# Kernel tuning notes

Hardware: AMD Instinct MI355X
Metric: run time of the kernel (lower is better)

Reference implementation:

```python
import jax, jax.numpy as jnp
import numpy as np

B, IN, H = 8192, 2048, 2048
EFF = IN + H  # self_recurrent concat of [x_t, state]


def setup_inputs() -> dict:
    key = jax.random.key(0)
    ks = jax.random.split(key, 6)
    s_in = 1.0 / np.sqrt(EFF).astype(np.float32)
    s_h = 1.0 / np.sqrt(H).astype(np.float32)
    return {
        "x_t": jax.random.normal(ks[0], (B, IN), jnp.float32),
        "state": jax.random.normal(ks[1], (B, H), jnp.float32),
        "Wc": jax.random.normal(ks[2], (EFF, H), jnp.float32) * s_in,
        "Uc": jax.random.normal(ks[3], (H, H), jnp.float32) * s_h,
        "bc": jnp.zeros((H,), jnp.float32),
        "Wg": jax.random.normal(ks[4], (EFF, H), jnp.float32) * s_in,
        "Ug": jax.random.normal(ks[5], (H, H), jnp.float32) * s_h,
        "bg": jnp.zeros((H,), jnp.float32),
        "log_step": jnp.zeros((H,), jnp.float32),  # dt_scale=1.0 -> no init shift
        "gamma": jnp.ones((H,), jnp.float32),
        "beta": jnp.zeros((H,), jnp.float32),
    }


def _layernorm(x, gamma, beta, eps=1e-5):
    mu = jnp.mean(x, axis=-1, keepdims=True)
    var = jnp.mean((x - mu) ** 2, axis=-1, keepdims=True)
    return (x - mu) * jax.lax.rsqrt(var + eps) * gamma + beta


def reference(x_t, state, Wc, Uc, bc, Wg, Ug, bg, log_step, gamma, beta):
    dt = 1.0  # step(dt=1.0) * dt_scale(1.0)
    xin = jnp.concatenate([x_t, state], axis=-1)        # [B, EFF], self_recurrent
    cand = jnp.tanh(xin @ Wc + state @ Uc + bc)          # candidate state [B, H]
    gate = jax.nn.sigmoid(xin @ Wg + state @ Ug + bg)    # input gate [B, H]
    tau = jnp.exp(log_step)                              # learned time constant
    alpha = jnp.exp(-dt / tau)                           # exp(-dt/tau) decay
    h_new = alpha * state + (1.0 - alpha) * gate * cand  # liquid gated update
    return _layernorm(h_new, gamma, beta)                # post-norm
```

## Files before the change

kernel.cpp:

```cpp
#include <hip/hip_runtime.h>
#include <hip/hip_bf16.h>
#include <cstdint>
#include <cstddef>

#define Bsz 8192
#define Hdim 2048
#define Kdim 4096
#define Nall 4096

#define BM 128
#define BN 64
#define BK 32

typedef __attribute__((ext_vector_type(8))) short short8;
typedef __attribute__((ext_vector_type(4))) short short4v;
typedef __attribute__((ext_vector_type(4))) float floatx4;

__device__ __forceinline__ short f2bf(float f) {
    unsigned u = __float_as_uint(f);
    unsigned r = (u + 0x7fffu + ((u >> 16) & 1u)) >> 16;
    return (short)(r & 0xffffu);
}

__device__ __forceinline__ float fast_tanh(float x) {
    float e = __expf(2.f * x);
    return 1.f - 2.f / (e + 1.f);
}
__device__ __forceinline__ float fast_sigmoid(float x) {
    return 1.f / (1.f + __expf(-x));
}

__device__ __forceinline__ void g2l16(const void* g, void* l) {
    __builtin_amdgcn_global_load_lds(
        (const __attribute__((address_space(1))) unsigned int*)g,
        (__attribute__((address_space(3))) unsigned int*)l,
        16, 0, 0);
}

__global__ __launch_bounds__(256) void build_wt(
    const float* __restrict__ Wc, const float* __restrict__ Uc,
    const float* __restrict__ Wg, const float* __restrict__ Ug,
    short* __restrict__ Wt)
{
    __shared__ float tile[32][33];
    const int nt = blockIdx.x * 32;
    const int kt = blockIdx.y * 32;
    const int tx = threadIdx.x & 31;
    const int ty = threadIdx.x >> 5;

    const bool isGate = (nt >= Hdim);
    const float* W = isGate ? Wg : Wc;
    const float* U = isGate ? Ug : Uc;
    const int ncol = isGate ? (nt - Hdim) : nt;

#pragma unroll
    for (int r = 0; r < 32; r += 8) {
        int k = kt + ty + r;
        float v = W[(size_t)k * Hdim + ncol + tx];
        if (k >= Hdim) v += U[(size_t)(k - Hdim) * Hdim + ncol + tx];
        tile[ty + r][tx] = v;
    }
    __syncthreads();
    const int nrow = threadIdx.x >> 3;
    const int kg   = threadIdx.x & 7;
    short4v o;
#pragma unroll
    for (int i = 0; i < 4; ++i) o[i] = f2bf(tile[kg * 4 + i][nrow]);
    *(short4v*)&Wt[(size_t)(nt + nrow) * Kdim + kt + kg * 4] = o;
}

__global__ __launch_bounds__(256) void build_acat(
    const float* __restrict__ x, const float* __restrict__ st,
    short* __restrict__ A)
{
    int idx = blockIdx.x * 256 + threadIdx.x;
    int row = idx >> 9;
    int c = (idx & 511) * 8;
    const float* src = (c < Hdim) ? (x + (size_t)row * Hdim + c)
                                  : (st + (size_t)row * Hdim + (c - Hdim));
    float4 v0 = ((const float4*)src)[0];
    float4 v1 = ((const float4*)src)[1];
    short8 o;
    o[0] = f2bf(v0.x); o[1] = f2bf(v0.y); o[2] = f2bf(v0.z); o[3] = f2bf(v0.w);
    o[4] = f2bf(v1.x); o[5] = f2bf(v1.y); o[6] = f2bf(v1.z); o[7] = f2bf(v1.w);
    *(short8*)(A + (size_t)row * Kdim + c) = o;
}

__global__ __launch_bounds__(256, 2) void gemm_fused(
    const short* __restrict__ A,
    const short* __restrict__ Bt,
    const float* __restrict__ st,
    const float* __restrict__ bc, const float* __restrict__ bg,
    const float* __restrict__ lstep,
    float* __restrict__ Hout)
{
    __shared__ __attribute__((aligned(16))) short sA [BM * BK];
    __shared__ __attribute__((aligned(16))) short sBc[BN * BK];
    __shared__ __attribute__((aligned(16))) short sBg[BN * BK];

    const int tid  = threadIdx.x;
    const int lane = tid & 63;
    const int wave = tid >> 6;
    const int wm = wave >> 1;
    const int wn = wave & 1;

    const int m0 = blockIdx.y * BM;
    const int n0 = blockIdx.x * BN;
    const int K = Kdim;

    floatx4 accc[4][2], accg[4][2];
#pragma unroll
    for (int i = 0; i < 4; ++i)
#pragma unroll
        for (int j = 0; j < 2; ++j) {
            floatx4 z = {0.f, 0.f, 0.f, 0.f};
            accc[i][j] = z; accg[i][j] = z;
        }

    const int r0 = tid >> 2;
    const int c0 = ((tid & 3) ^ ((r0 >> 1) & 3)) * 8;
    const short* Ag0 = A  + (size_t)(m0 + r0)        * K + c0;
    const short* Ag1 = A  + (size_t)(m0 + 64 + r0)   * K + c0;
    const short* Bc0 = Bt + (size_t)(n0 + r0)        * K + c0;
    const short* Bg0 = Bt + (size_t)(Hdim + n0 + r0) * K + c0;

    short* dA0 = sA  + wave * 512;
    short* dA1 = sA  + 2048 + wave * 512;
    short* dBc = sBc + wave * 512;
    short* dBg = sBg + wave * 512;

    const int fr = lane & 15;
    const int j4 = lane >> 4;
    const int rslot = (j4 ^ ((fr >> 1) & 3)) * 8;
    const short* sAf  = sA  + (wm * 64 + fr) * BK + rslot;
    const short* sBcf = sBc + (wn * 32 + fr) * BK + rslot;
    const short* sBgf = sBg + (wn * 32 + fr) * BK + rslot;

    for (int k0 = 0; k0 < K; k0 += BK) {
        __syncthreads();
        g2l16(Ag0, dA0); g2l16(Ag1, dA1);
        g2l16(Bc0, dBc); g2l16(Bg0, dBg);
        Ag0 += BK; Ag1 += BK; Bc0 += BK; Bg0 += BK;
        __syncthreads();

        short8 a[4], bcf[2], bgf[2];
#pragma unroll
        for (int i = 0; i < 4; ++i) a[i] = *(const short8*)(sAf + i * 16 * BK);
#pragma unroll
        for (int j = 0; j < 2; ++j) {
            bcf[j] = *(const short8*)(sBcf + j * 16 * BK);
            bgf[j] = *(const short8*)(sBgf + j * 16 * BK);
        }
#pragma unroll
        for (int i = 0; i < 4; ++i)
#pragma unroll
            for (int j = 0; j < 2; ++j) {
                accc[i][j] = __builtin_amdgcn_mfma_f32_16x16x32_bf16(
                    a[i], bcf[j], accc[i][j], 0, 0, 0);
                accg[i][j] = __builtin_amdgcn_mfma_f32_16x16x32_bf16(
                    a[i], bgf[j], accg[i][j], 0, 0, 0);
            }
    }

    const int cn = lane & 15;
    const int cr = (lane >> 4) * 4;
    float bcv[2], bgv[2], alv[2];
#pragma unroll
    for (int j = 0; j < 2; ++j) {
        int col = n0 + wn * 32 + j * 16 + cn;
        bcv[j] = bc[col];
        bgv[j] = bg[col];
        alv[j] = __expf(-__expf(-lstep[col]));
    }
#pragma unroll
    for (int i = 0; i < 4; ++i) {
        int rowb = m0 + wm * 64 + i * 16 + cr;
#pragma unroll
        for (int r = 0; r < 4; ++r) {
            int row = rowb + r;
            const float* sp = st + (size_t)row * Hdim;
            float* hp = Hout + (size_t)row * Hdim;
#pragma unroll
            for (int j = 0; j < 2; ++j) {
                int col = n0 + wn * 32 + j * 16 + cn;
                float cand = fast_tanh(accc[i][j][r] + bcv[j]);
                float gate = fast_sigmoid(accg[i][j][r] + bgv[j]);
                float al = alv[j];
                hp[col] = al * sp[col] + (1.f - al) * gate * cand;
            }
        }
    }
}

__global__ __launch_bounds__(256) void ln_k(
    const float* __restrict__ h, const float* __restrict__ gam,
    const float* __restrict__ bet, float* __restrict__ out)
{
    const int b = blockIdx.x;
    const int t = threadIdx.x;
    const int n0 = t * 8;
    const float* hp = h + (size_t)b * Hdim + n0;

    float4 v0 = ((const float4*)hp)[0];
    float4 v1 = ((const float4*)hp)[1];
    float hv[8] = {v0.x, v0.y, v0.z, v0.w, v1.x, v1.y, v1.z, v1.w};
    float sum = 0.f, ss = 0.f;
#pragma unroll
    for (int i = 0; i < 8; ++i) { sum += hv[i]; ss += hv[i] * hv[i]; }

#pragma unroll
    for (int off = 32; off > 0; off >>= 1) {
        sum += __shfl_down(sum, off);
        ss  += __shfl_down(ss, off);
    }
    __shared__ float red[2][4];
    if ((t & 63) == 0) { red[0][t >> 6] = sum; red[1][t >> 6] = ss; }
    __syncthreads();
    sum = red[0][0] + red[0][1] + red[0][2] + red[0][3];
    ss  = red[1][0] + red[1][1] + red[1][2] + red[1][3];

    const float inv = 1.f / (float)Hdim;
    float mu = sum * inv;
    float var = ss * inv - mu * mu;
    float rs = rsqrtf(var + 1e-5f);

    float* op = out + (size_t)b * Hdim + n0;
#pragma unroll
    for (int i = 0; i < 8; ++i) {
        int n = n0 + i;
        op[i] = (hv[i] - mu) * rs * gam[n] + bet[n];
    }
}

extern "C" void kernel_launch(void* const* d_in, const int* in_sizes, int n_in,
                              void* d_out, int out_size, void* d_ws, size_t ws_size,
                              hipStream_t stream)
{
    const float* x_t   = (const float*)d_in[0];
    const float* state = (const float*)d_in[1];
    const float* Wc    = (const float*)d_in[2];
    const float* Uc    = (const float*)d_in[3];
    const float* bc    = (const float*)d_in[4];
    const float* Wg    = (const float*)d_in[5];
    const float* Ug    = (const float*)d_in[6];
    const float* bg    = (const float*)d_in[7];
    const float* lstep = (const float*)d_in[8];
    const float* gam   = (const float*)d_in[9];
    const float* bet   = (const float*)d_in[10];
    float* out = (float*)d_out;

    char* ws = (char*)d_ws;
    short* Wt   = (short*)ws;
    short* Acat = (short*)(ws + (size_t)32 * 1024 * 1024);
    float* h    = (float*)(ws + (size_t)96 * 1024 * 1024);

    build_wt<<<dim3(Nall / 32, Kdim / 32), 256, 0, stream>>>(Wc, Uc, Wg, Ug, Wt);
    build_acat<<<(Bsz * (Kdim / 8)) / 256, 256, 0, stream>>>(x_t, state, Acat);
    gemm_fused<<<dim3(Hdim / BN, Bsz / BM), 256, 0, stream>>>(
        Acat, Wt, state, bc, bg, lstep, h);
    ln_k<<<Bsz, 256, 0, stream>>>(h, gam, bet, out);
}
```

Measured before the change: 581.7 us.

## Store intermediate h in bf16, reuse bf16 state from Acat, remap blocks per XCD

The fused GEMM epilogue now reads the recurrent state from the bf16 Acat buffer instead of the fp32 input. It writes the pre-norm h as bf16 instead of fp32, and the layernorm kernel reads bf16. This halves intermediate traffic in the epilogue and the LN pass. The 1D grid is also remapped so each XCD handles a contiguous band of M tiles, which should improve L2 reuse of A. The cost is precision: both the state term alpha*state and h are rounded to bf16 before the layernorm.

```diff
diff --git a/kernel.cpp b/kernel.cpp
--- a/kernel.cpp
+++ b/kernel.cpp
@@ -20,6 +20,9 @@
     unsigned u = __float_as_uint(f);
     unsigned r = (u + 0x7fffu + ((u >> 16) & 1u)) >> 16;
     return (short)(r & 0xffffu);
+}
+__device__ __forceinline__ float bf2f(short b) {
+    return __uint_as_float(((unsigned)(unsigned short)b) << 16);
 }
 
 __device__ __forceinline__ float fast_tanh(float x) {
@@ -89,10 +92,9 @@
 __global__ __launch_bounds__(256, 2) void gemm_fused(
     const short* __restrict__ A,
     const short* __restrict__ Bt,
-    const float* __restrict__ st,
     const float* __restrict__ bc, const float* __restrict__ bg,
     const float* __restrict__ lstep,
-    float* __restrict__ Hout)
+    short* __restrict__ Hout)
 {
     __shared__ __attribute__((aligned(16))) short sA [BM * BK];
     __shared__ __attribute__((aligned(16))) short sBc[BN * BK];
@@ -104,8 +106,13 @@
     const int wm = wave >> 1;
     const int wn = wave & 1;
 
-    const int m0 = blockIdx.y * BM;
-    const int n0 = blockIdx.x * BN;
+    const int bidx = blockIdx.x;
+    const int xcd = bidx & 7;
+    const int q   = bidx >> 3;
+    const int nb  = q & 31;
+    const int mb  = xcd * 8 + (q >> 5);
+    const int m0 = mb * BM;
+    const int n0 = nb * BN;
     const int K = Kdim;
 
     floatx4 accc[4][2], accg[4][2];
@@ -178,35 +185,37 @@
 #pragma unroll
         for (int r = 0; r < 4; ++r) {
             int row = rowb + r;
-            const float* sp = st + (size_t)row * Hdim;
-            float* hp = Hout + (size_t)row * Hdim;
+            const short* sp = A + (size_t)row * Kdim + Hdim;
+            short* hp = Hout + (size_t)row * Hdim;
 #pragma unroll
             for (int j = 0; j < 2; ++j) {
                 int col = n0 + wn * 32 + j * 16 + cn;
                 float cand = fast_tanh(accc[i][j][r] + bcv[j]);
                 float gate = fast_sigmoid(accg[i][j][r] + bgv[j]);
                 float al = alv[j];
-                hp[col] = al * sp[col] + (1.f - al) * gate * cand;
+                float hv = al * bf2f(sp[col]) + (1.f - al) * gate * cand;
+                hp[col] = f2bf(hv);
             }
         }
     }
 }
 
 __global__ __launch_bounds__(256) void ln_k(
-    const float* __restrict__ h, const float* __restrict__ gam,
+    const short* __restrict__ h, const float* __restrict__ gam,
     const float* __restrict__ bet, float* __restrict__ out)
 {
     const int b = blockIdx.x;
     const int t = threadIdx.x;
     const int n0 = t * 8;
-    const float* hp = h + (size_t)b * Hdim + n0;
-
-    float4 v0 = ((const float4*)hp)[0];
-    float4 v1 = ((const float4*)hp)[1];
-    float hv[8] = {v0.x, v0.y, v0.z, v0.w, v1.x, v1.y, v1.z, v1.w};
+    short8 hb = *(const short8*)(h + (size_t)b * Hdim + n0);
+
+    float hv[8];
     float sum = 0.f, ss = 0.f;
 #pragma unroll
-    for (int i = 0; i < 8; ++i) { sum += hv[i]; ss += hv[i] * hv[i]; }
+    for (int i = 0; i < 8; ++i) {
+        hv[i] = bf2f(hb[i]);
+        sum += hv[i]; ss += hv[i] * hv[i];
+    }
 
 #pragma unroll
     for (int off = 32; off > 0; off >>= 1) {
@@ -252,11 +261,11 @@
     char* ws = (char*)d_ws;
     short* Wt   = (short*)ws;
     short* Acat = (short*)(ws + (size_t)32 * 1024 * 1024);
-    float* h    = (float*)(ws + (size_t)96 * 1024 * 1024);
+    short* h    = (short*)(ws + (size_t)96 * 1024 * 1024);
 
     build_wt<<<dim3(Nall / 32, Kdim / 32), 256, 0, stream>>>(Wc, Uc, Wg, Ug, Wt);
     build_acat<<<(Bsz * (Kdim / 8)) / 256, 256, 0, stream>>>(x_t, state, Acat);
-    gemm_fused<<<dim3(Hdim / BN, Bsz / BM), 256, 0, stream>>>(
-        Acat, Wt, state, bc, bg, lstep, h);
+    gemm_fused<<<(Bsz / BM) * (Hdim / BN), 256, 0, stream>>>(
+        Acat, Wt, bc, bg, lstep, h);
     ln_k<<<Bsz, 256, 0, stream>>>(h, gam, bet, out);
 }
```

After: 602.2 us. 3.5% more time.
